# Optimization experiments

Hardware: AMD Instinct MI355X
Metric: run time of the kernel (lower is better)

## Reference

```python
import jax, jax.numpy as jnp
import numpy as np

DS_DIM = 2
N_EXPERTS = 64
N_CLASSES = 26
IMG = 68
BATCH = 8192
FLAT = 1960  # 10 * 14 * 14 after two conv+pool stages


def _conv2d(x, w, b):
    # x: [B, Cin, H, W], w: [Cout, Cin, kh, kw]
    y = jax.lax.conv_general_dilated(
        x, w, window_strides=(1, 1), padding='VALID',
        dimension_numbers=('NCHW', 'OIHW', 'NCHW'))
    return y + b[None, :, None, None]


def _maxpool2(x):
    return jax.lax.reduce_window(
        x, -jnp.inf, jax.lax.max,
        window_dimensions=(1, 1, 2, 2), window_strides=(1, 1, 2, 2),
        padding='VALID')


def setup_inputs() -> dict:
    key = jax.random.key(0)
    ks = jax.random.split(key, 14)
    x = jax.random.normal(ks[0], (BATCH, DS_DIM), dtype=jnp.float32)
    cls_idx = jax.random.randint(ks[1], (BATCH,), 0, N_CLASSES)
    images = jax.random.normal(ks[2], (N_CLASSES, 1, IMG, IMG), dtype=jnp.float32)
    s = 0.05
    conv1_w = jax.random.normal(ks[3], (5, 1, 5, 5), dtype=jnp.float32) * s
    conv1_b = jax.random.normal(ks[4], (5,), dtype=jnp.float32) * s
    conv2_w = jax.random.normal(ks[5], (10, 5, 5, 5), dtype=jnp.float32) * s
    conv2_b = jax.random.normal(ks[6], (10,), dtype=jnp.float32) * s
    fc1_w = jax.random.normal(ks[7], (500, FLAT + DS_DIM), dtype=jnp.float32) * s
    fc1_b = jax.random.normal(ks[8], (500,), dtype=jnp.float32) * s
    fc2_w = jax.random.normal(ks[9], (N_EXPERTS, 500), dtype=jnp.float32) * s
    fc2_b = jax.random.normal(ks[10], (N_EXPERTS,), dtype=jnp.float32) * s
    # geotorch-constrained expert matrices: B_A positive-semidefinite, C_A skew
    raw_b = jax.random.normal(ks[11], (N_EXPERTS, DS_DIM, DS_DIM), dtype=jnp.float32)
    A_B = jnp.einsum('nik,njk->nij', raw_b, raw_b) * 0.1        # PSD
    raw_c = jax.random.normal(ks[12], (N_EXPERTS, DS_DIM, DS_DIM), dtype=jnp.float32)
    A_C = (raw_c - jnp.swapaxes(raw_c, -1, -2)) * 0.5            # skew
    x_tar = jax.random.normal(ks[13], (1, DS_DIM), dtype=jnp.float32)
    return {'x': x, 'cls_idx': cls_idx, 'images': images,
            'conv1_w': conv1_w, 'conv1_b': conv1_b,
            'conv2_w': conv2_w, 'conv2_b': conv2_b,
            'fc1_w': fc1_w, 'fc1_b': fc1_b,
            'fc2_w': fc2_w, 'fc2_b': fc2_b,
            'A_B': A_B, 'A_C': A_C, 'x_tar': x_tar}


def reference(x, cls_idx, images, conv1_w, conv1_b, conv2_w, conv2_b,
              fc1_w, fc1_b, fc2_w, fc2_b, A_B, A_C, x_tar):
    # gating CNN: gather per-sample image by class index
    img = images[cls_idx]                             # [B, 1, 68, 68]
    h = _maxpool2(jax.nn.relu(_conv2d(img, conv1_w, conv1_b)))   # [B, 5, 32, 32]
    h = _maxpool2(jax.nn.relu(_conv2d(h, conv2_w, conv2_b)))     # [B, 10, 14, 14]
    h = h.reshape(h.shape[0], -1)                     # [B, 1960]
    h = jnp.concatenate([h, x], axis=1)               # [B, 1962]
    h = jax.nn.relu(h @ fc1_w.T + fc1_b)              # [B, 500]
    w_all = jax.nn.softmax(h @ fc2_w.T + fc2_b, axis=1)  # [B, N]
    # fused expert weighted-sum (original: python loop over N tiny matmuls)
    A = A_B + A_C                                     # [N, d, d]
    diff = x_tar - x                                  # [B, d]
    s_all = jnp.einsum('bn,nij,bj->bi', w_all, A, diff)
    return s_all
```

## Files before the change

### kernel.cpp

```cpp
#include <hip/hip_runtime.h>

#define WS_SC1    0
#define WS_FEAT   133120
#define WS_FC1P   184080
#define WS_FC2P   197080
#define WS_AFLAT  229080
#define WS_WX     229336

__global__ __launch_bounds__(256) void k_conv1(
    const float* __restrict__ images, const float* __restrict__ c1w,
    const float* __restrict__ c1b, const float* __restrict__ fc2w,
    const float* __restrict__ fc1w, const float* __restrict__ A_B,
    const float* __restrict__ A_C, float* __restrict__ ws)
{
    const int b = blockIdx.x, t = threadIdx.x;
    if (b >= 520) {
        if (b == 520) {
            float* P = ws + WS_FC2P;
            for (int i = t; i < 8000; i += 256) {
                int j4 = i >> 6, e = i & 63;
                float4 v;
                v.x = fc2w[e * 500 + 4 * j4 + 0];
                v.y = fc2w[e * 500 + 4 * j4 + 1];
                v.z = fc2w[e * 500 + 4 * j4 + 2];
                v.w = fc2w[e * 500 + 4 * j4 + 3];
                *(float4*)&P[i * 4] = v;
            }
        } else {
            float* Af = ws + WS_AFLAT;
            if (t < 256) Af[t] = A_B[t] + A_C[t];
            float* Wx = ws + WS_WX;
            for (int i = t; i < 1000; i += 256) {
                int j = i >> 1, k = i & 1;
                Wx[i] = fc1w[j * 1962 + 1960 + k];
            }
        }
        return;
    }

    const int c = b / 20, r = b - c * 20;
    const int oc = r >> 2, g = r & 3;
    const int py = g * 8 + (t >> 5), px = t & 31;

    float wr[25];
#pragma unroll
    for (int i = 0; i < 25; ++i) wr[i] = c1w[oc * 25 + i];
    const float bias = c1b[oc];

    const float* im = images + c * 4624 + (2 * py) * 68 + 2 * px;
    float ir[6][6];
#pragma unroll
    for (int a = 0; a < 6; ++a)
#pragma unroll
        for (int q = 0; q < 3; ++q) {
            float2 v = *(const float2*)&im[a * 68 + 2 * q];
            ir[a][2 * q] = v.x; ir[a][2 * q + 1] = v.y;
        }

    float a00 = bias, a01 = bias, a10 = bias, a11 = bias;
#pragma unroll
    for (int ky = 0; ky < 5; ++ky)
#pragma unroll
        for (int kx = 0; kx < 5; ++kx) {
            float w = wr[ky * 5 + kx];
            a00 += w * ir[ky][kx];     a01 += w * ir[ky][kx + 1];
            a10 += w * ir[ky + 1][kx]; a11 += w * ir[ky + 1][kx + 1];
        }
    float v = fmaxf(fmaxf(fmaxf(a00, a01), fmaxf(a10, a11)), 0.f);
    ws[WS_SC1 + ((c * 5 + oc) * 32 + py) * 32 + px] = v;
}

__global__ __launch_bounds__(256) void k_conv2(
    const float* __restrict__ c2w, const float* __restrict__ c2b,
    float* __restrict__ ws)
{
    const int b = blockIdx.x, t = threadIdx.x;
    const int c = b / 10, oc = b - c * 10;

    __shared__ float sw[125];
    if (t < 125) sw[t] = c2w[oc * 125 + t];
    __syncthreads();
    if (t >= 196) return;

    const int py = t / 14, px = t - py * 14;
    const float bias = c2b[oc];
    float a00 = bias, a01 = bias, a10 = bias, a11 = bias;

    const float* base = ws + WS_SC1 + c * 5120 + (2 * py) * 32 + 2 * px;
#pragma unroll
    for (int ic = 0; ic < 5; ++ic) {
        const float* s1 = base + ic * 1024;
        float ir[6][6];
#pragma unroll
        for (int a = 0; a < 6; ++a)
#pragma unroll
            for (int q = 0; q < 3; ++q) {
                float2 v = *(const float2*)&s1[a * 32 + 2 * q];
                ir[a][2 * q] = v.x; ir[a][2 * q + 1] = v.y;
            }
#pragma unroll
        for (int ky = 0; ky < 5; ++ky)
#pragma unroll
            for (int kx = 0; kx < 5; ++kx) {
                float w = sw[ic * 25 + ky * 5 + kx];
                a00 += w * ir[ky][kx];     a01 += w * ir[ky][kx + 1];
                a10 += w * ir[ky + 1][kx]; a11 += w * ir[ky + 1][kx + 1];
            }
    }
    float v = fmaxf(fmaxf(fmaxf(a00, a01), fmaxf(a10, a11)), 0.f);
    ws[WS_FEAT + c * 1960 + oc * 196 + py * 14 + px] = v;
}

__global__ __launch_bounds__(256) void k_fc1(
    const float* __restrict__ fc1w, const float* __restrict__ fc1b,
    float* __restrict__ ws)
{
    const int lane = threadIdx.x & 63, w = threadIdx.x >> 6;
    const int c = blockIdx.x / 63, jg = blockIdx.x - c * 63;
    const int j0 = jg * 8 + 2 * w;
    if (j0 >= 500) return;
    const int j1 = j0 + 1;

    const float* f  = ws + WS_FEAT + c * 1960;
    const float* w0 = fc1w + j0 * 1962;
    const float* w1 = fc1w + j1 * 1962;

    float acc0 = 0.f, acc1 = 0.f;
#pragma unroll
    for (int i = 0; i < 30; ++i) {
        int k = lane + 64 * i;
        float fv = f[k];
        acc0 += w0[k] * fv;
        acc1 += w1[k] * fv;
    }
    {
        int k = lane + 1920;
        if (k < 1960) {
            float fv = f[k];
            acc0 += w0[k] * fv;
            acc1 += w1[k] * fv;
        }
    }
#pragma unroll
    for (int off = 32; off >= 1; off >>= 1) {
        acc0 += __shfl_xor(acc0, off);
        acc1 += __shfl_xor(acc1, off);
    }
    if (lane == 0) {
        ws[WS_FC1P + c * 500 + j0] = acc0 + fc1b[j0];
        ws[WS_FC1P + c * 500 + j1] = acc1 + fc1b[j1];
    }
}

__global__ __launch_bounds__(256) void k_moe(
    const float* __restrict__ x, const int* __restrict__ cls,
    const float* __restrict__ fc2b, const float* __restrict__ x_tar,
    const float* __restrict__ ws, float* __restrict__ out)
{
    __shared__ float sh[8][500];
    __shared__ float sred[2048];
    const int t = threadIdx.x;
    const int b0 = blockIdx.x * 8;
    const float* fc1p = ws + WS_FC1P;
    const float* fc2P = ws + WS_FC2P;
    const float* Af   = ws + WS_AFLAT;
    const float* Wx   = ws + WS_WX;

    int cs[8]; float xs0[8], xs1[8];
#pragma unroll
    for (int s = 0; s < 8; ++s) {
        cs[s]  = cls[b0 + s];
        xs0[s] = x[2 * (b0 + s)];
        xs1[s] = x[2 * (b0 + s) + 1];
    }
    for (int j = t; j < 500; j += 256) {
        float2 wx = *(const float2*)&Wx[2 * j];
#pragma unroll
        for (int s = 0; s < 8; ++s) {
            float v = fc1p[cs[s] * 500 + j] + xs0[s] * wx.x + xs1[s] * wx.y;
            sh[s][j] = fmaxf(v, 0.f);
        }
    }
    __syncthreads();

    const int e = t & 63, p = t >> 6;
    float acc[8];
#pragma unroll
    for (int s = 0; s < 8; ++s) acc[s] = 0.f;

    const int gbeg = p * 32;
    const int gend = (p == 3) ? 125 : (gbeg + 32);
    for (int j4 = gbeg; j4 < gend; ++j4) {
        float4 wv = *(const float4*)&fc2P[(j4 * 64 + e) * 4];
#pragma unroll
        for (int s = 0; s < 8; ++s) {
            float4 h4 = *(const float4*)&sh[s][j4 * 4];
            acc[s] += h4.x * wv.x + h4.y * wv.y + h4.z * wv.z + h4.w * wv.w;
        }
    }
#pragma unroll
    for (int s = 0; s < 8; ++s) sred[p * 512 + s * 64 + e] = acc[s];
    __syncthreads();

    const float xt0 = x_tar[0], xt1 = x_tar[1];
    const float be = fc2b[e];
    const float4 a4 = *(const float4*)&Af[4 * e];
#pragma unroll
    for (int half = 0; half < 2; ++half) {
        int s = half * 4 + p;
        float logit = be + sred[s * 64 + e] + sred[512 + s * 64 + e]
                    + sred[1024 + s * 64 + e] + sred[1536 + s * 64 + e];
        float m = logit;
#pragma unroll
        for (int off = 32; off >= 1; off >>= 1) m = fmaxf(m, __shfl_xor(m, off));
        float ex = __expf(logit - m);
        float sum = ex;
        float m0 = ex * a4.x, m1 = ex * a4.y, m2 = ex * a4.z, m3 = ex * a4.w;
#pragma unroll
        for (int off = 32; off >= 1; off >>= 1) {
            sum += __shfl_xor(sum, off);
            m0 += __shfl_xor(m0, off);
            m1 += __shfl_xor(m1, off);
            m2 += __shfl_xor(m2, off);
            m3 += __shfl_xor(m3, off);
        }
        if (e == 0) {
            int bb = b0 + s;
            float d0 = xt0 - x[2 * bb], d1 = xt1 - x[2 * bb + 1];
            float inv = 1.f / sum;
            out[2 * bb]     = (m0 * d0 + m1 * d1) * inv;
            out[2 * bb + 1] = (m2 * d0 + m3 * d1) * inv;
        }
    }
}

extern "C" void kernel_launch(void* const* d_in, const int* in_sizes, int n_in,
                              void* d_out, int out_size, void* d_ws, size_t ws_size,
                              hipStream_t stream) {
    const float* x      = (const float*)d_in[0];
    const int*   cls    = (const int*)  d_in[1];
    const float* images = (const float*)d_in[2];
    const float* c1w    = (const float*)d_in[3];
    const float* c1b    = (const float*)d_in[4];
    const float* c2w    = (const float*)d_in[5];
    const float* c2b    = (const float*)d_in[6];
    const float* fc1w   = (const float*)d_in[7];
    const float* fc1b   = (const float*)d_in[8];
    const float* fc2w   = (const float*)d_in[9];
    const float* fc2b   = (const float*)d_in[10];
    const float* A_B    = (const float*)d_in[11];
    const float* A_C    = (const float*)d_in[12];
    const float* x_tar  = (const float*)d_in[13];
    float* out = (float*)d_out;
    float* ws  = (float*)d_ws;

    k_conv1<<<522, 256, 0, stream>>>(images, c1w, c1b, fc2w, fc1w, A_B, A_C, ws);
    k_conv2<<<260, 256, 0, stream>>>(c2w, c2b, ws);
    k_fc1  <<<1638, 256, 0, stream>>>(fc1w, fc1b, ws);
    k_moe  <<<1024, 256, 0, stream>>>(x, cls, fc2b, x_tar, ws, out);
}
```

Measured before the change: 129.5 us.

## Split MoE kernel into hidden-activation pass and register-resident fc2 logits pass

Splits the fused MoE kernel into two kernels. k_h materializes the ReLU'd fc1 hidden activations for every sample into global workspace. k_logits keeps each wave's slice of fc2 weights in a per-thread register array and streams 16 samples' hidden rows from global memory before the softmax and expert sum. The aim is to reuse fc2 weights from registers instead of refetching them per 8-sample block. In exchange it adds a roughly 16 MB global write and read of H, an extra launch, and a dynamically indexed register array that may spill to scratch.

```diff
diff --git a/kernel.cpp b/kernel.cpp
--- a/kernel.cpp
+++ b/kernel.cpp
@@ -6,6 +6,7 @@
 #define WS_FC2P   197080
 #define WS_AFLAT  229080
 #define WS_WX     229336
+#define WS_H      262144
 
 __global__ __launch_bounds__(256) void k_conv1(
     const float* __restrict__ images, const float* __restrict__ c1w,
@@ -152,64 +153,73 @@
     }
 }
 
-__global__ __launch_bounds__(256) void k_moe(
+__global__ __launch_bounds__(256) void k_h(
     const float* __restrict__ x, const int* __restrict__ cls,
-    const float* __restrict__ fc2b, const float* __restrict__ x_tar,
-    const float* __restrict__ ws, float* __restrict__ out)
-{
-    __shared__ float sh[8][500];
-    __shared__ float sred[2048];
+    float* __restrict__ ws)
+{
     const int t = threadIdx.x;
     const int b0 = blockIdx.x * 8;
     const float* fc1p = ws + WS_FC1P;
+    const float* Wx   = ws + WS_WX;
+    float* H = ws + WS_H;
+
+#pragma unroll
+    for (int s = 0; s < 8; ++s) {
+        const int b = b0 + s;
+        const int c = cls[b];
+        const float x0 = x[2 * b], x1 = x[2 * b + 1];
+        const float* fr = fc1p + c * 500;
+        float* hr = H + (size_t)b * 500;
+        for (int j2 = t; j2 < 250; j2 += 256) {
+            float2 f  = *(const float2*)&fr[2 * j2];
+            float4 wx = *(const float4*)&Wx[4 * j2];
+            float h0 = fmaxf(f.x + x0 * wx.x + x1 * wx.y, 0.f);
+            float h1 = fmaxf(f.y + x0 * wx.z + x1 * wx.w, 0.f);
+            *(float2*)&hr[2 * j2] = make_float2(h0, h1);
+        }
+    }
+}
+
+__global__ __launch_bounds__(256) void k_logits(
+    const float* __restrict__ x, const float* __restrict__ fc2b,
+    const float* __restrict__ x_tar, const float* __restrict__ ws,
+    float* __restrict__ out)
+{
+    __shared__ float sred[4096];
+    const int t = threadIdx.x;
+    const int e = t & 63;
+    const int pu = __builtin_amdgcn_readfirstlane(t >> 6);
+    const int b0 = blockIdx.x * 16;
+    const float* H    = ws + WS_H;
     const float* fc2P = ws + WS_FC2P;
     const float* Af   = ws + WS_AFLAT;
-    const float* Wx   = ws + WS_WX;
-
-    int cs[8]; float xs0[8], xs1[8];
-#pragma unroll
-    for (int s = 0; s < 8; ++s) {
-        cs[s]  = cls[b0 + s];
-        xs0[s] = x[2 * (b0 + s)];
-        xs1[s] = x[2 * (b0 + s) + 1];
-    }
-    for (int j = t; j < 500; j += 256) {
-        float2 wx = *(const float2*)&Wx[2 * j];
-#pragma unroll
-        for (int s = 0; s < 8; ++s) {
-            float v = fc1p[cs[s] * 500 + j] + xs0[s] * wx.x + xs1[s] * wx.y;
-            sh[s][j] = fmaxf(v, 0.f);
-        }
-    }
-    __syncthreads();
-
-    const int e = t & 63, p = t >> 6;
-    float acc[8];
-#pragma unroll
-    for (int s = 0; s < 8; ++s) acc[s] = 0.f;
-
-    const int gbeg = p * 32;
-    const int gend = (p == 3) ? 125 : (gbeg + 32);
-    for (int j4 = gbeg; j4 < gend; ++j4) {
-        float4 wv = *(const float4*)&fc2P[(j4 * 64 + e) * 4];
-#pragma unroll
-        for (int s = 0; s < 8; ++s) {
-            float4 h4 = *(const float4*)&sh[s][j4 * 4];
-            acc[s] += h4.x * wv.x + h4.y * wv.y + h4.z * wv.z + h4.w * wv.w;
-        }
-    }
-#pragma unroll
-    for (int s = 0; s < 8; ++s) sred[p * 512 + s * 64 + e] = acc[s];
+
+    const int jbeg4 = pu * 32;
+    const int jcnt4 = (pu == 3) ? 29 : 32;
+
+    float4 w[32];
+    for (int i = 0; i < jcnt4; ++i)
+        w[i] = *(const float4*)&fc2P[((jbeg4 + i) * 64 + e) * 4];
+
+    for (int s = 0; s < 16; ++s) {
+        const float* hrow = H + (size_t)(b0 + s) * 500 + jbeg4 * 4;
+        float a = 0.f;
+        for (int i = 0; i < jcnt4; ++i) {
+            float4 h4 = *(const float4*)&hrow[4 * i];
+            a += h4.x * w[i].x + h4.y * w[i].y + h4.z * w[i].z + h4.w * w[i].w;
+        }
+        sred[(pu * 16 + s) * 64 + e] = a;
+    }
     __syncthreads();
 
     const float xt0 = x_tar[0], xt1 = x_tar[1];
     const float be = fc2b[e];
     const float4 a4 = *(const float4*)&Af[4 * e];
 #pragma unroll
-    for (int half = 0; half < 2; ++half) {
-        int s = half * 4 + p;
-        float logit = be + sred[s * 64 + e] + sred[512 + s * 64 + e]
-                    + sred[1024 + s * 64 + e] + sred[1536 + s * 64 + e];
+    for (int k = 0; k < 4; ++k) {
+        const int s = pu * 4 + k;
+        float logit = be + sred[s * 64 + e] + sred[(16 + s) * 64 + e]
+                    + sred[(32 + s) * 64 + e] + sred[(48 + s) * 64 + e];
         float m = logit;
 #pragma unroll
         for (int off = 32; off >= 1; off >>= 1) m = fmaxf(m, __shfl_xor(m, off));
@@ -225,11 +235,11 @@
             m3 += __shfl_xor(m3, off);
         }
         if (e == 0) {
-            int bb = b0 + s;
-            float d0 = xt0 - x[2 * bb], d1 = xt1 - x[2 * bb + 1];
+            const int b = b0 + s;
+            float d0 = xt0 - x[2 * b], d1 = xt1 - x[2 * b + 1];
             float inv = 1.f / sum;
-            out[2 * bb]     = (m0 * d0 + m1 * d1) * inv;
-            out[2 * bb + 1] = (m2 * d0 + m3 * d1) * inv;
+            out[2 * b]     = (m0 * d0 + m1 * d1) * inv;
+            out[2 * b + 1] = (m2 * d0 + m3 * d1) * inv;
         }
     }
 }
@@ -254,8 +264,9 @@
     float* out = (float*)d_out;
     float* ws  = (float*)d_ws;
 
-    k_conv1<<<522, 256, 0, stream>>>(images, c1w, c1b, fc2w, fc1w, A_B, A_C, ws);
-    k_conv2<<<260, 256, 0, stream>>>(c2w, c2b, ws);
-    k_fc1  <<<1638, 256, 0, stream>>>(fc1w, fc1b, ws);
-    k_moe  <<<1024, 256, 0, stream>>>(x, cls, fc2b, x_tar, ws, out);
-}
+    k_conv1 <<<522, 256, 0, stream>>>(images, c1w, c1b, fc2w, fc1w, A_B, A_C, ws);
+    k_conv2 <<<260, 256, 0, stream>>>(c2w, c2b, ws);
+    k_fc1   <<<1638, 256, 0, stream>>>(fc1w, fc1b, ws);
+    k_h     <<<1024, 256, 0, stream>>>(x, cls, ws);
+    k_logits<<<512, 256, 0, stream>>>(x, fc2b, x_tar, ws, out);
+}
```

Result: slower. 309.2 us (+138.7%).
